# Optimization experiments

Measured on AMD Instinct MI355X. Metric: run time of the kernel, lower is better.

## Reference

```python
import jax, jax.numpy as jnp
import numpy as np

HIDDEN_DIM = 2048
NUM_EXPERTS = 64
TOP_K = 2
NUM_TOKENS = 16384


def setup_inputs() -> dict:
    key = jax.random.key(0)
    kx, kw, kb = jax.random.split(key, 3)
    X = jax.random.normal(kx, (NUM_TOKENS, HIDDEN_DIM), dtype=jnp.float32)
    # nn.Linear(hidden_dim, num_experts): weight [num_experts, hidden_dim], bias [num_experts]
    bound = 1.0 / np.sqrt(HIDDEN_DIM)
    W = jax.random.uniform(kw, (NUM_EXPERTS, HIDDEN_DIM), minval=-bound, maxval=bound, dtype=jnp.float32)
    b = jax.random.uniform(kb, (NUM_EXPERTS,), minval=-bound, maxval=bound, dtype=jnp.float32)
    return {"X": X, "W": W, "b": b}


def reference(X, W, b):
    # router_logits = gate(X): [T, E]
    router_logits = jnp.einsum("th,eh->te", X, W) + b
    # softmax in float32 (matches dtype=torch.float)
    routing_probs = jax.nn.softmax(router_logits.astype(jnp.float32), axis=-1)
    # top-k over experts: [T, K]
    router_weights, selected_experts = jax.lax.top_k(routing_probs, TOP_K)
    # renormalize over selected experts (sum cast to X.dtype, result stays fp32 math)
    denom = jnp.sum(router_weights, axis=-1, keepdims=True).astype(X.dtype)
    router_weights = router_weights / denom
    # one-hot expert mask: [T, K, E], int64 like F.one_hot
    expert_mask = jax.nn.one_hot(selected_experts, NUM_EXPERTS, dtype=jnp.int32)
    return (router_logits, router_weights, selected_experts, expert_mask)
```

## Files before the change

kernel.cpp:

```cpp
#include <hip/hip_runtime.h>
#include <math.h>

constexpr int T_TOK = 16384;
constexpr int HDIM  = 2048;
constexpr int NEXP  = 64;
constexpr int TPB   = 32;
constexpr int MT    = TPB / 16;
constexpr int NWAVE = 8;
constexpr int KPW   = HDIM / NWAVE;
constexpr int KSTEP = 32;
constexpr int NKS   = KPW / KSTEP;

typedef __attribute__((ext_vector_type(8))) short v8s;
typedef __attribute__((ext_vector_type(4))) float v4f;

#define MFMA_BF16 __builtin_amdgcn_mfma_f32_16x16x32_bf16

static __device__ __forceinline__ void split3(float x, unsigned short& h,
                                              unsigned short& m, unsigned short& l)
{
    unsigned u0 = __float_as_uint(x);
    h = (unsigned short)(u0 >> 16);
    float r1 = x - __uint_as_float(u0 & 0xFFFF0000u);
    unsigned u1 = __float_as_uint(r1);
    m = (unsigned short)(u1 >> 16);
    float r2 = r1 - __uint_as_float(u1 & 0xFFFF0000u);
    l = (unsigned short)(__float_as_uint(r2) >> 16);
}

static __device__ __forceinline__ void frag3(const float4& x0, const float4& x1,
                                             v8s& h, v8s& m, v8s& l)
{
    unsigned short sh, sm, sl;
    split3(x0.x, sh, sm, sl); h[0]=(short)sh; m[0]=(short)sm; l[0]=(short)sl;
    split3(x0.y, sh, sm, sl); h[1]=(short)sh; m[1]=(short)sm; l[1]=(short)sl;
    split3(x0.z, sh, sm, sl); h[2]=(short)sh; m[2]=(short)sm; l[2]=(short)sl;
    split3(x0.w, sh, sm, sl); h[3]=(short)sh; m[3]=(short)sm; l[3]=(short)sl;
    split3(x1.x, sh, sm, sl); h[4]=(short)sh; m[4]=(short)sm; l[4]=(short)sl;
    split3(x1.y, sh, sm, sl); h[5]=(short)sh; m[5]=(short)sm; l[5]=(short)sl;
    split3(x1.z, sh, sm, sl); h[6]=(short)sh; m[6]=(short)sm; l[6]=(short)sl;
    split3(x1.w, sh, sm, sl); h[7]=(short)sh; m[7]=(short)sm; l[7]=(short)sl;
}

static __device__ __forceinline__ int swz_e(int tok, int e) {
    return e ^ (((tok >> 2) & 1) << 4);
}

__global__ __launch_bounds__(512, 4)
void moe_router_mfma(const float* __restrict__ X,
                     const float* __restrict__ Wg,
                     const float* __restrict__ Bg,
                     float* __restrict__ out)
{
    __shared__ float red[4][TPB][NEXP];

    const int tid  = threadIdx.x;
    const int lane = tid & 63;
    const int wv   = tid >> 6;
    const int r16  = lane & 15;
    const int q    = lane >> 4;
    const int tok0 = blockIdx.x * TPB;

    const float* pA = X  + (size_t)(tok0 + r16) * HDIM + wv * KPW + q * 8;
    const float* pB = Wg + (size_t)r16 * HDIM + wv * KPW + q * 8;

    v4f acc[MT][4];
#pragma unroll
    for (int mt = 0; mt < MT; ++mt)
#pragma unroll
        for (int nt = 0; nt < 4; ++nt)
            acc[mt][nt] = (v4f){0.f, 0.f, 0.f, 0.f};

    float4 a0[MT], a1[MT], b0[4], b1[4];
#pragma unroll
    for (int mt = 0; mt < MT; ++mt) {
        const float* p = pA + (size_t)mt * 16 * HDIM;
        a0[mt] = *(const float4*)p;
        a1[mt] = *(const float4*)(p + 4);
    }
#pragma unroll
    for (int nt = 0; nt < 4; ++nt) {
        const float* p = pB + (size_t)nt * 16 * HDIM;
        b0[nt] = *(const float4*)p;
        b1[nt] = *(const float4*)(p + 4);
    }

    for (int ks = 0; ks < NKS; ++ks) {
        v8s Ah[MT], Am[MT], Al[MT], Bh[4], Bm[4], Bl[4];
#pragma unroll
        for (int mt = 0; mt < MT; ++mt) frag3(a0[mt], a1[mt], Ah[mt], Am[mt], Al[mt]);
#pragma unroll
        for (int nt = 0; nt < 4; ++nt) frag3(b0[nt], b1[nt], Bh[nt], Bm[nt], Bl[nt]);

        if (ks < NKS - 1) {
            const int off = (ks + 1) * KSTEP;
#pragma unroll
            for (int mt = 0; mt < MT; ++mt) {
                const float* p = pA + (size_t)mt * 16 * HDIM + off;
                a0[mt] = *(const float4*)p;
                a1[mt] = *(const float4*)(p + 4);
            }
#pragma unroll
            for (int nt = 0; nt < 4; ++nt) {
                const float* p = pB + (size_t)nt * 16 * HDIM + off;
                b0[nt] = *(const float4*)p;
                b1[nt] = *(const float4*)(p + 4);
            }
        }

#pragma unroll
        for (int mt = 0; mt < MT; ++mt)
#pragma unroll
            for (int nt = 0; nt < 4; ++nt) {
                v4f a = acc[mt][nt];
                a = MFMA_BF16(Ah[mt], Bh[nt], a, 0, 0, 0);
                a = MFMA_BF16(Ah[mt], Bm[nt], a, 0, 0, 0);
                a = MFMA_BF16(Am[mt], Bh[nt], a, 0, 0, 0);
                a = MFMA_BF16(Ah[mt], Bl[nt], a, 0, 0, 0);
                a = MFMA_BF16(Al[mt], Bh[nt], a, 0, 0, 0);
                a = MFMA_BF16(Am[mt], Bm[nt], a, 0, 0, 0);
                acc[mt][nt] = a;
            }
    }

    if (wv < 4) {
#pragma unroll
        for (int mt = 0; mt < MT; ++mt)
#pragma unroll
            for (int nt = 0; nt < 4; ++nt)
#pragma unroll
                for (int r = 0; r < 4; ++r) {
                    int tok = 16 * mt + q * 4 + r;
                    int e   = 16 * nt + r16;
                    red[wv][tok][swz_e(tok, e)] = acc[mt][nt][r];
                }
    }
    __syncthreads();
    if (wv >= 4) {
#pragma unroll
        for (int mt = 0; mt < MT; ++mt)
#pragma unroll
            for (int nt = 0; nt < 4; ++nt)
#pragma unroll
                for (int r = 0; r < 4; ++r) {
                    int tok = 16 * mt + q * 4 + r;
                    int e   = 16 * nt + r16;
                    red[wv - 4][tok][swz_e(tok, e)] += acc[mt][nt][r];
                }
    }
    __syncthreads();

    if (lane < 4) {
        const int tk = wv * 4 + lane;
        const int t  = tok0 + tk;
        const int sh = lane << 4;
        float lg[NEXP];
#pragma unroll
        for (int eo = 0; eo < NEXP; ++eo) {
            int e  = (eo + sh) & (NEXP - 1);
            int es = swz_e(tk, e);
            lg[eo] = ((red[0][tk][es] + red[1][tk][es]) +
                      (red[2][tk][es] + red[3][tk][es])) + Bg[e];
        }
        float* outL = out + (size_t)t * NEXP;
#pragma unroll
        for (int eo = 0; eo < NEXP; eo += 4) {
            int e = (eo + sh) & (NEXP - 1);
            float4 v = make_float4(lg[eo], lg[eo+1], lg[eo+2], lg[eo+3]);
            *(float4*)(outL + e) = v;
        }
        float mx = lg[0];
#pragma unroll
        for (int eo = 1; eo < NEXP; ++eo) mx = fmaxf(mx, lg[eo]);
        float S = 0.f;
#pragma unroll
        for (int eo = 0; eo < NEXP; ++eo) { lg[eo] = expf(lg[eo] - mx); S += lg[eo]; }
#pragma unroll
        for (int eo = 0; eo < NEXP; ++eo) lg[eo] = lg[eo] / S;

        float v1 = lg[0]; int i1o = 0;
        float v2 = -1.0f; int i2o = 0;
#pragma unroll
        for (int eo = 1; eo < NEXP; ++eo) {
            float rv = lg[eo];
            bool g1 = rv > v1;
            bool g2 = rv > v2;
            float nv2 = g1 ? v1 : (g2 ? rv : v2);
            int   ni2 = g1 ? i1o : (g2 ? eo : i2o);
            v2 = nv2; i2o = ni2;
            v1 = g1 ? rv : v1;
            i1o = g1 ? eo : i1o;
        }
        const int i1 = (i1o + sh) & (NEXP - 1);
        const int i2 = (i2o + sh) & (NEXP - 1);
        float den = v1 + v2;
        float w1 = v1 / den, w2 = v2 / den;

        float* outW = out + (size_t)T_TOK * NEXP;
        float* outS = outW + (size_t)T_TOK * 2;
        float* outM = outS + (size_t)T_TOK * 2;
        outW[2*t+0] = w1;        outW[2*t+1] = w2;
        outS[2*t+0] = (float)i1; outS[2*t+1] = (float)i2;

        float* mrow = outM + (size_t)t * 2 * NEXP;
#pragma unroll
        for (int e = 0; e < NEXP; e += 4) {
            float4 a = make_float4(e+0==i1?1.f:0.f, e+1==i1?1.f:0.f,
                                   e+2==i1?1.f:0.f, e+3==i1?1.f:0.f);
            *(float4*)(mrow + e) = a;
            float4 b = make_float4(e+0==i2?1.f:0.f, e+1==i2?1.f:0.f,
                                   e+2==i2?1.f:0.f, e+3==i2?1.f:0.f);
            *(float4*)(mrow + NEXP + e) = b;
        }
    }
}

extern "C" void kernel_launch(void* const* d_in, const int* in_sizes, int n_in,
                              void* d_out, int out_size, void* d_ws, size_t ws_size,
                              hipStream_t stream)
{
    const float* X = (const float*)d_in[0];
    const float* W = (const float*)d_in[1];
    const float* B = (const float*)d_in[2];
    float* out     = (float*)d_out;

    dim3 grid(T_TOK / TPB);
    dim3 block(512);
    hipLaunchKernelGGL(moe_router_mfma, grid, block, 0, stream, X, W, B, out);
}
```

Baseline: 263.2 us.

## Pre-split gate weights into bf16 triplets in a separate kernel

Adds a small pre-pass kernel that splits the fp32 gate weights once into high/mid/low bf16 planes in workspace, so the main kernel loads ready-made B fragments instead of re-splitting W in every block. The main loop is fully unrolled and interleaves B loads in two halves between MFMA groups. This removes redundant per-block ALU split work on W, at the cost of an extra launch, workspace traffic and potentially exposed load latency since B is no longer prefetched a step ahead.

Result: no change. 268.4 us (+2.0%).

```diff
diff --git a/kernel.cpp b/kernel.cpp
--- a/kernel.cpp
+++ b/kernel.cpp
@@ -46,9 +46,28 @@
     return e ^ (((tok >> 2) & 1) << 4);
 }
 
+__global__ __launch_bounds__(256)
+void split_w_kernel(const float* __restrict__ W,
+                    short* __restrict__ Wh,
+                    short* __restrict__ Wm,
+                    short* __restrict__ Wl)
+{
+    const int idx = blockIdx.x * 256 + threadIdx.x;
+    const float* p = W + (size_t)idx * 8;
+    float4 x0 = *(const float4*)p;
+    float4 x1 = *(const float4*)(p + 4);
+    v8s h, m, l;
+    frag3(x0, x1, h, m, l);
+    *(v8s*)(Wh + (size_t)idx * 8) = h;
+    *(v8s*)(Wm + (size_t)idx * 8) = m;
+    *(v8s*)(Wl + (size_t)idx * 8) = l;
+}
+
 __global__ __launch_bounds__(512, 4)
 void moe_router_mfma(const float* __restrict__ X,
-                     const float* __restrict__ Wg,
+                     const short* __restrict__ Wh,
+                     const short* __restrict__ Wm,
+                     const short* __restrict__ Wl,
                      const float* __restrict__ Bg,
                      float* __restrict__ out)
 {
@@ -61,8 +80,8 @@
     const int q    = lane >> 4;
     const int tok0 = blockIdx.x * TPB;
 
-    const float* pA = X  + (size_t)(tok0 + r16) * HDIM + wv * KPW + q * 8;
-    const float* pB = Wg + (size_t)r16 * HDIM + wv * KPW + q * 8;
+    const float* pA = X + (size_t)(tok0 + r16) * HDIM + wv * KPW + q * 8;
+    const int ob = r16 * HDIM + wv * KPW + q * 8;
 
     v4f acc[MT][4];
 #pragma unroll
@@ -71,26 +90,28 @@
         for (int nt = 0; nt < 4; ++nt)
             acc[mt][nt] = (v4f){0.f, 0.f, 0.f, 0.f};
 
-    float4 a0[MT], a1[MT], b0[4], b1[4];
+    float4 a0[MT], a1[MT];
 #pragma unroll
     for (int mt = 0; mt < MT; ++mt) {
         const float* p = pA + (size_t)mt * 16 * HDIM;
         a0[mt] = *(const float4*)p;
         a1[mt] = *(const float4*)(p + 4);
     }
-#pragma unroll
-    for (int nt = 0; nt < 4; ++nt) {
-        const float* p = pB + (size_t)nt * 16 * HDIM;
-        b0[nt] = *(const float4*)p;
-        b1[nt] = *(const float4*)(p + 4);
-    }
-
+
+#pragma unroll
     for (int ks = 0; ks < NKS; ++ks) {
-        v8s Ah[MT], Am[MT], Al[MT], Bh[4], Bm[4], Bl[4];
+        const int ke = ob + ks * KSTEP;
+
+        v8s Bh0 = *(const v8s*)(Wh + ke);
+        v8s Bm0 = *(const v8s*)(Wm + ke);
+        v8s Bl0 = *(const v8s*)(Wl + ke);
+        v8s Bh1 = *(const v8s*)(Wh + 32768 + ke);
+        v8s Bm1 = *(const v8s*)(Wm + 32768 + ke);
+        v8s Bl1 = *(const v8s*)(Wl + 32768 + ke);
+
+        v8s Ah[MT], Am[MT], Al[MT];
 #pragma unroll
         for (int mt = 0; mt < MT; ++mt) frag3(a0[mt], a1[mt], Ah[mt], Am[mt], Al[mt]);
-#pragma unroll
-        for (int nt = 0; nt < 4; ++nt) frag3(b0[nt], b1[nt], Bh[nt], Bm[nt], Bl[nt]);
 
         if (ks < NKS - 1) {
             const int off = (ks + 1) * KSTEP;
@@ -100,27 +121,54 @@
                 a0[mt] = *(const float4*)p;
                 a1[mt] = *(const float4*)(p + 4);
             }
-#pragma unroll
-            for (int nt = 0; nt < 4; ++nt) {
-                const float* p = pB + (size_t)nt * 16 * HDIM + off;
-                b0[nt] = *(const float4*)p;
-                b1[nt] = *(const float4*)(p + 4);
-            }
-        }
-
-#pragma unroll
-        for (int mt = 0; mt < MT; ++mt)
-#pragma unroll
-            for (int nt = 0; nt < 4; ++nt) {
-                v4f a = acc[mt][nt];
-                a = MFMA_BF16(Ah[mt], Bh[nt], a, 0, 0, 0);
-                a = MFMA_BF16(Ah[mt], Bm[nt], a, 0, 0, 0);
-                a = MFMA_BF16(Am[mt], Bh[nt], a, 0, 0, 0);
-                a = MFMA_BF16(Ah[mt], Bl[nt], a, 0, 0, 0);
-                a = MFMA_BF16(Al[mt], Bh[nt], a, 0, 0, 0);
-                a = MFMA_BF16(Am[mt], Bm[nt], a, 0, 0, 0);
-                acc[mt][nt] = a;
-            }
+        }
+
+#pragma unroll
+        for (int mt = 0; mt < MT; ++mt) {
+            v4f a = acc[mt][0];
+            a = MFMA_BF16(Ah[mt], Bh0, a, 0, 0, 0);
+            a = MFMA_BF16(Ah[mt], Bm0, a, 0, 0, 0);
+            a = MFMA_BF16(Am[mt], Bh0, a, 0, 0, 0);
+            a = MFMA_BF16(Ah[mt], Bl0, a, 0, 0, 0);
+            a = MFMA_BF16(Al[mt], Bh0, a, 0, 0, 0);
+            a = MFMA_BF16(Am[mt], Bm0, a, 0, 0, 0);
+            acc[mt][0] = a;
+            v4f b = acc[mt][1];
+            b = MFMA_BF16(Ah[mt], Bh1, b, 0, 0, 0);
+            b = MFMA_BF16(Ah[mt], Bm1, b, 0, 0, 0);
+            b = MFMA_BF16(Am[mt], Bh1, b, 0, 0, 0);
+            b = MFMA_BF16(Ah[mt], Bl1, b, 0, 0, 0);
+            b = MFMA_BF16(Al[mt], Bh1, b, 0, 0, 0);
+            b = MFMA_BF16(Am[mt], Bm1, b, 0, 0, 0);
+            acc[mt][1] = b;
+        }
+
+        v8s Bh2 = *(const v8s*)(Wh + 2 * 32768 + ke);
+        v8s Bm2 = *(const v8s*)(Wm + 2 * 32768 + ke);
+        v8s Bl2 = *(const v8s*)(Wl + 2 * 32768 + ke);
+        v8s Bh3 = *(const v8s*)(Wh + 3 * 32768 + ke);
+        v8s Bm3 = *(const v8s*)(Wm + 3 * 32768 + ke);
+        v8s Bl3 = *(const v8s*)(Wl + 3 * 32768 + ke);
+
+#pragma unroll
+        for (int mt = 0; mt < MT; ++mt) {
+            v4f a = acc[mt][2];
+            a = MFMA_BF16(Ah[mt], Bh2, a, 0, 0, 0);
+            a = MFMA_BF16(Ah[mt], Bm2, a, 0, 0, 0);
+            a = MFMA_BF16(Am[mt], Bh2, a, 0, 0, 0);
+            a = MFMA_BF16(Ah[mt], Bl2, a, 0, 0, 0);
+            a = MFMA_BF16(Al[mt], Bh2, a, 0, 0, 0);
+            a = MFMA_BF16(Am[mt], Bm2, a, 0, 0, 0);
+            acc[mt][2] = a;
+            v4f b = acc[mt][3];
+            b = MFMA_BF16(Ah[mt], Bh3, b, 0, 0, 0);
+            b = MFMA_BF16(Ah[mt], Bm3, b, 0, 0, 0);
+            b = MFMA_BF16(Am[mt], Bh3, b, 0, 0, 0);
+            b = MFMA_BF16(Ah[mt], Bl3, b, 0, 0, 0);
+            b = MFMA_BF16(Al[mt], Bh3, b, 0, 0, 0);
+            b = MFMA_BF16(Am[mt], Bm3, b, 0, 0, 0);
+            acc[mt][3] = b;
+        }
     }
 
     if (wv < 4) {
@@ -224,7 +272,12 @@
     const float* B = (const float*)d_in[2];
     float* out     = (float*)d_out;
 
-    dim3 grid(T_TOK / TPB);
-    dim3 block(512);
-    hipLaunchKernelGGL(moe_router_mfma, grid, block, 0, stream, X, W, B, out);
-}
+    short* Wh = (short*)d_ws;
+    short* Wm = Wh + NEXP * HDIM;
+    short* Wl = Wm + NEXP * HDIM;
+
+    hipLaunchKernelGGL(split_w_kernel, dim3(NEXP * HDIM / 8 / 256), dim3(256),
+                       0, stream, W, Wh, Wm, Wl);
+    hipLaunchKernelGGL(moe_router_mfma, dim3(T_TOK / TPB), dim3(512),
+                       0, stream, X, Wh, Wm, Wl, B, out);
+}
```

## Pre-split W into bf16 fragments and stage X via LDS with double buffering

Applied to the files above, without the earlier changes.

A new pre-pass kernel splits W once per call into packed bf16 hi/mid/lo MFMA fragments in the workspace, so the main kernel no longer re-splits W in every block. The main kernel moves from a split-K layout, where each wave covered all 64 experts over a K slice, to one where each wave owns a 16x16 token-by-expert tile over the full K. X tiles are streamed into swizzled, double-buffered LDS with global_load_lds, and the cross-wave partial-sum reduction is removed. This trades per-block W conversion and reduction work for an extra launch, workspace traffic, and a __syncthreads on every K step.

Result: faster. 254.4 us (-3.3%).

```diff
diff --git a/kernel.cpp b/kernel.cpp
--- a/kernel.cpp
+++ b/kernel.cpp
@@ -5,11 +5,8 @@
 constexpr int HDIM  = 2048;
 constexpr int NEXP  = 64;
 constexpr int TPB   = 32;
-constexpr int MT    = TPB / 16;
-constexpr int NWAVE = 8;
-constexpr int KPW   = HDIM / NWAVE;
-constexpr int KSTEP = 32;
-constexpr int NKS   = KPW / KSTEP;
+constexpr int KSTEP = 64;
+constexpr int NK    = HDIM / KSTEP;
 
 typedef __attribute__((ext_vector_type(8))) short v8s;
 typedef __attribute__((ext_vector_type(4))) float v4f;
@@ -46,107 +43,128 @@
     return e ^ (((tok >> 2) & 1) << 4);
 }
 
+static __device__ __forceinline__ void glds16(const float* g, float* l)
+{
+    __builtin_amdgcn_global_load_lds((const __attribute__((address_space(1))) void*)g,
+                                     (__attribute__((address_space(3))) void*)l,
+                                     16, 0, 0);
+}
+
+__global__ __launch_bounds__(256)
+void pack_w_kernel(const float* __restrict__ W, short* __restrict__ P)
+{
+    const int tid = blockIdx.x * 256 + threadIdx.x;
+    const int l   = tid & 63;
+    int g = tid >> 6;
+    const int p  = g % 3;  g /= 3;
+    const int nt = g % 4;  g /= 4;
+    const int ks32 = g;
+    const int r16 = l & 15, q = l >> 4;
+    const float* src = W + (size_t)(nt * 16 + r16) * HDIM + ks32 * 32 + q * 8;
+    float4 x0 = *(const float4*)src;
+    float4 x1 = *(const float4*)(src + 4);
+    v8s h, m, lo;
+    frag3(x0, x1, h, m, lo);
+    v8s outv = (p == 0) ? h : (p == 1) ? m : lo;
+    *(v8s*)(P + (size_t)tid * 8) = outv;
+}
+
+#define BLOAD(ks32, p) (*(const v8s*)(pB + ((size_t)(ks32) * 12 + (p)) * 512))
+
+#define COMPUTE(CUR, B0,B1,B2,B3,B4,B5)                                   \
+    do {                                                                  \
+        float4 x0 = *(const float4*)&smem[(CUR) + ap00];                  \
+        float4 x1 = *(const float4*)&smem[(CUR) + ap01];                  \
+        v8s Ah, Am, Al;                                                   \
+        frag3(x0, x1, Ah, Am, Al);                                        \
+        acc = MFMA_BF16(Ah, B0, acc, 0, 0, 0);                            \
+        acc = MFMA_BF16(Ah, B1, acc, 0, 0, 0);                            \
+        acc = MFMA_BF16(Am, B0, acc, 0, 0, 0);                            \
+        acc = MFMA_BF16(Ah, B2, acc, 0, 0, 0);                            \
+        acc = MFMA_BF16(Al, B0, acc, 0, 0, 0);                            \
+        acc = MFMA_BF16(Am, B1, acc, 0, 0, 0);                            \
+        float4 y0 = *(const float4*)&smem[(CUR) + ap10];                  \
+        float4 y1 = *(const float4*)&smem[(CUR) + ap11];                  \
+        frag3(y0, y1, Ah, Am, Al);                                        \
+        acc = MFMA_BF16(Ah, B3, acc, 0, 0, 0);                            \
+        acc = MFMA_BF16(Ah, B4, acc, 0, 0, 0);                            \
+        acc = MFMA_BF16(Am, B3, acc, 0, 0, 0);                            \
+        acc = MFMA_BF16(Ah, B5, acc, 0, 0, 0);                            \
+        acc = MFMA_BF16(Al, B3, acc, 0, 0, 0);                            \
+        acc = MFMA_BF16(Am, B4, acc, 0, 0, 0);                            \
+    } while (0)
+
 __global__ __launch_bounds__(512, 4)
 void moe_router_mfma(const float* __restrict__ X,
-                     const float* __restrict__ Wg,
+                     const short* __restrict__ Pw,
                      const float* __restrict__ Bg,
                      float* __restrict__ out)
 {
-    __shared__ float red[4][TPB][NEXP];
+    __shared__ __align__(16) float smem[8192];
 
     const int tid  = threadIdx.x;
     const int lane = tid & 63;
     const int wv   = tid >> 6;
+    const int wn   = wv & 3;
+    const int wm   = wv >> 2;
     const int r16  = lane & 15;
     const int q    = lane >> 4;
     const int tok0 = blockIdx.x * TPB;
 
-    const float* pA = X  + (size_t)(tok0 + r16) * HDIM + wv * KPW + q * 8;
-    const float* pB = Wg + (size_t)r16 * HDIM + wv * KPW + q * 8;
-
-    v4f acc[MT][4];
-#pragma unroll
-    for (int mt = 0; mt < MT; ++mt)
-#pragma unroll
-        for (int nt = 0; nt < 4; ++nt)
-            acc[mt][nt] = (v4f){0.f, 0.f, 0.f, 0.f};
-
-    float4 a0[MT], a1[MT], b0[4], b1[4];
-#pragma unroll
-    for (int mt = 0; mt < MT; ++mt) {
-        const float* p = pA + (size_t)mt * 16 * HDIM;
-        a0[mt] = *(const float4*)p;
-        a1[mt] = *(const float4*)(p + 4);
+    const int srow   = wv * 4 + (lane >> 4);
+    const int schunk = (lane & 15) ^ (srow & 7);
+    const float* gA  = X + (size_t)(tok0 + srow) * HDIM + schunk * 4;
+    const int ldst   = wv * 256;
+
+    const int arow  = wm * 16 + r16;
+    const int abase = arow * 64;
+    const int sx    = arow & 7;
+    const int ap00  = abase + (((q * 2) + 0) ^ sx) * 4;
+    const int ap01  = abase + (((q * 2) + 1) ^ sx) * 4;
+    const int ap10  = abase + ((8 + (q * 2) + 0) ^ sx) * 4;
+    const int ap11  = abase + ((8 + (q * 2) + 1) ^ sx) * 4;
+
+    const short* pB = Pw + (size_t)(wn * 3) * 512 + lane * 8;
+
+    v4f acc = (v4f){0.f, 0.f, 0.f, 0.f};
+
+    glds16(gA, &smem[ldst]);
+    v8s Ba0 = BLOAD(0, 0), Ba1 = BLOAD(0, 1), Ba2 = BLOAD(0, 2);
+    v8s Ba3 = BLOAD(1, 0), Ba4 = BLOAD(1, 1), Ba5 = BLOAD(1, 2);
+    v8s Bb0, Bb1, Bb2, Bb3, Bb4, Bb5;
+    __syncthreads();
+
+    for (int ks2 = 0; ks2 < NK / 2; ++ks2) {
+        {
+            const int ksn = 2 * ks2 + 1;
+            glds16(gA + ksn * KSTEP, &smem[4096 + ldst]);
+            const int k32 = ksn * 2;
+            Bb0 = BLOAD(k32, 0); Bb1 = BLOAD(k32, 1); Bb2 = BLOAD(k32, 2);
+            Bb3 = BLOAD(k32 + 1, 0); Bb4 = BLOAD(k32 + 1, 1); Bb5 = BLOAD(k32 + 1, 2);
+            COMPUTE(0, Ba0, Ba1, Ba2, Ba3, Ba4, Ba5);
+            __syncthreads();
+        }
+        {
+            const int ksn = 2 * ks2 + 2;
+            if (ksn < NK) {
+                glds16(gA + ksn * KSTEP, &smem[ldst]);
+                const int k32 = ksn * 2;
+                Ba0 = BLOAD(k32, 0); Ba1 = BLOAD(k32, 1); Ba2 = BLOAD(k32, 2);
+                Ba3 = BLOAD(k32 + 1, 0); Ba4 = BLOAD(k32 + 1, 1); Ba5 = BLOAD(k32 + 1, 2);
+            }
+            COMPUTE(4096, Bb0, Bb1, Bb2, Bb3, Bb4, Bb5);
+            __syncthreads();
+        }
     }
-#pragma unroll
-    for (int nt = 0; nt < 4; ++nt) {
-        const float* p = pB + (size_t)nt * 16 * HDIM;
-        b0[nt] = *(const float4*)p;
-        b1[nt] = *(const float4*)(p + 4);
-    }
-
-    for (int ks = 0; ks < NKS; ++ks) {
-        v8s Ah[MT], Am[MT], Al[MT], Bh[4], Bm[4], Bl[4];
-#pragma unroll
-        for (int mt = 0; mt < MT; ++mt) frag3(a0[mt], a1[mt], Ah[mt], Am[mt], Al[mt]);
-#pragma unroll
-        for (int nt = 0; nt < 4; ++nt) frag3(b0[nt], b1[nt], Bh[nt], Bm[nt], Bl[nt]);
-
-        if (ks < NKS - 1) {
-            const int off = (ks + 1) * KSTEP;
-#pragma unroll
-            for (int mt = 0; mt < MT; ++mt) {
-                const float* p = pA + (size_t)mt * 16 * HDIM + off;
-                a0[mt] = *(const float4*)p;
-                a1[mt] = *(const float4*)(p + 4);
-            }
-#pragma unroll
-            for (int nt = 0; nt < 4; ++nt) {
-                const float* p = pB + (size_t)nt * 16 * HDIM + off;
-                b0[nt] = *(const float4*)p;
-                b1[nt] = *(const float4*)(p + 4);
-            }
-        }
-
-#pragma unroll
-        for (int mt = 0; mt < MT; ++mt)
-#pragma unroll
-            for (int nt = 0; nt < 4; ++nt) {
-                v4f a = acc[mt][nt];
-                a = MFMA_BF16(Ah[mt], Bh[nt], a, 0, 0, 0);
-                a = MFMA_BF16(Ah[mt], Bm[nt], a, 0, 0, 0);
-                a = MFMA_BF16(Am[mt], Bh[nt], a, 0, 0, 0);
-                a = MFMA_BF16(Ah[mt], Bl[nt], a, 0, 0, 0);
-                a = MFMA_BF16(Al[mt], Bh[nt], a, 0, 0, 0);
-                a = MFMA_BF16(Am[mt], Bm[nt], a, 0, 0, 0);
-                acc[mt][nt] = a;
-            }
-    }
-
-    if (wv < 4) {
-#pragma unroll
-        for (int mt = 0; mt < MT; ++mt)
-#pragma unroll
-            for (int nt = 0; nt < 4; ++nt)
-#pragma unroll
-                for (int r = 0; r < 4; ++r) {
-                    int tok = 16 * mt + q * 4 + r;
-                    int e   = 16 * nt + r16;
-                    red[wv][tok][swz_e(tok, e)] = acc[mt][nt][r];
-                }
-    }
-    __syncthreads();
-    if (wv >= 4) {
-#pragma unroll
-        for (int mt = 0; mt < MT; ++mt)
-#pragma unroll
-            for (int nt = 0; nt < 4; ++nt)
-#pragma unroll
-                for (int r = 0; r < 4; ++r) {
-                    int tok = 16 * mt + q * 4 + r;
-                    int e   = 16 * nt + r16;
-                    red[wv - 4][tok][swz_e(tok, e)] += acc[mt][nt][r];
-                }
+
+    float (*red)[NEXP] = (float (*)[NEXP])smem;
+    {
+        const int e = wn * 16 + r16;
+#pragma unroll
+        for (int r = 0; r < 4; ++r) {
+            int tok = wm * 16 + q * 4 + r;
+            red[tok][swz_e(tok, e)] = acc[r];
+        }
     }
     __syncthreads();
 
@@ -158,9 +176,7 @@
 #pragma unroll
         for (int eo = 0; eo < NEXP; ++eo) {
             int e  = (eo + sh) & (NEXP - 1);
-            int es = swz_e(tk, e);
-            lg[eo] = ((red[0][tk][es] + red[1][tk][es]) +
-                      (red[2][tk][es] + red[3][tk][es])) + Bg[e];
+            lg[eo] = red[tk][swz_e(tk, e)] + Bg[e];
         }
         float* outL = out + (size_t)t * NEXP;
 #pragma unroll
@@ -224,7 +240,10 @@
     const float* B = (const float*)d_in[2];
     float* out     = (float*)d_out;
 
-    dim3 grid(T_TOK / TPB);
-    dim3 block(512);
-    hipLaunchKernelGGL(moe_router_mfma, grid, block, 0, stream, X, W, B, out);
-}
+    short* Pw = (short*)d_ws;
+
+    hipLaunchKernelGGL(pack_w_kernel, dim3(49152 / 256), dim3(256),
+                       0, stream, W, Pw);
+    hipLaunchKernelGGL(moe_router_mfma, dim3(T_TOK / TPB), dim3(512),
+                       0, stream, X, Pw, B, out);
+}
```
